# Optimization experiments

Measured on AMD Instinct MI355X. Metric: run time of the kernel, lower is better.

Reference implementation:

```python
import jax, jax.numpy as jnp
import numpy as np

BLOCK_SIZE = 32
BLOCK_COUNTS = 8
N_MAX = 1024  # max seq len across jagged batch (static)
LN_EPS = 1e-5


def _silu(x):
    return x * jax.nn.sigmoid(x)


def setup_inputs() -> dict:
    key = jax.random.key(0)
    ks = jax.random.split(key, 5)
    T, H, D = 3200, 8, 128
    lengths = np.array([1024, 768, 896, 512], dtype=np.int64)
    offsets = np.concatenate([[0], np.cumsum(lengths)]).astype(np.int64)  # [B+1]
    q = jax.random.normal(ks[0], (T, H, D), jnp.float32)
    k = jax.random.normal(ks[1], (T, H, D), jnp.float32)
    v = jax.random.normal(ks[2], (T, H, D), jnp.float32)
    u = jax.random.normal(ks[3], (T, H, D), jnp.float32)
    Wg = jax.random.normal(ks[4], (H, D, 3), jnp.float32) * 0.05
    bg = jnp.zeros((H, 3), jnp.float32)
    return {"q": q, "k": k, "v": v, "u": u, "Wg": Wg, "bg": bg,
            "x_offsets": jnp.asarray(offsets)}


def _to_padded(jag, offsets, lengths, n):
    # jag: [T, H, D] -> [B, n, H, D], zero padded
    pos = jnp.arange(n)
    idx = offsets[:-1, None] + pos[None, :]                # [B, n]
    valid = pos[None, :] < lengths[:, None]                # [B, n]
    g = jag[jnp.clip(idx, 0, jag.shape[0] - 1)]            # [B, n, H, D]
    return jnp.where(valid[..., None, None], g, 0.0)


def _to_jagged(padded, offsets, T):
    tok = jnp.arange(T)
    b = jnp.searchsorted(offsets, tok, side='right') - 1   # batch id per token
    m = tok - offsets[b]                                   # local position
    return padded[b, m]


def _forward(q, k, v, u, Wg, bg, x_offsets):
    T, H, D = q.shape
    B = x_offsets.shape[0] - 1
    n = N_MAX
    bs = BLOCK_SIZE
    nb = n // bs
    S = min(BLOCK_COUNTS, nb)
    scale = D ** (-0.5)
    lengths = x_offsets[1:] - x_offsets[:-1]

    qp = _to_padded(q, x_offsets, lengths, n)  # [B, n, H, D]
    kp = _to_padded(k, x_offsets, lengths, n)
    vp = _to_padded(v, x_offsets, lengths, n)

    # gate model: per-head linear D->3 + sigmoid
    gates = jax.nn.sigmoid(jnp.einsum('bmhd,hde->bmhe', qp, Wg) + bg)
    g_cmp, g_slc = gates[..., 0], gates[..., 1]  # [B, n, H]

    # --- block compression ---
    k_cmp = kp.reshape(B, nb, bs, H, D).mean(axis=2)  # [B, nb, H, D]
    v_cmp = vp.reshape(B, nb, bs, H, D).mean(axis=2)

    # --- compressed attention + top-k block selection ---
    scores = jnp.einsum('bmhd,bkhd->bhmk', qp, k_cmp) * scale  # [B, H, n, nb]
    qblk = jnp.arange(n) // bs
    causal = qblk[:, None] >= jnp.arange(nb)[None, :]          # [n, nb]
    masked_scores = jnp.where(causal[None, None], scores, -jnp.inf)
    _, topk = jax.lax.top_k(masked_scores, S)                  # [B, H, n, S]
    topk = jnp.where(topk > qblk[None, None, :, None], -1, topk)

    p_cmp = jnp.where(causal[None, None], _silu(scores), 0.0)
    o_cmp = jnp.einsum('bhmk,bkhd->bmhd', p_cmp, v_cmp) * g_cmp[..., None]

    # --- selected (gathered top-k block) attention ---
    topk_p = jnp.transpose(topk, (0, 2, 1, 3))                 # [B, n, H, S]
    Kb = kp.reshape(B, nb, bs, H, D).transpose(0, 1, 3, 2, 4)  # [B, nb, H, bs, D]
    Vb = vp.reshape(B, nb, bs, H, D).transpose(0, 1, 3, 2, 4)
    b_ix = jnp.arange(B)[:, None, None]
    h_ix = jnp.arange(H)[None, None, :]
    m_pos = jnp.arange(n)
    off = jnp.arange(bs)

    def body(acc, s_idx):
        blk = jnp.take(topk_p, s_idx, axis=3)                  # [B, n, H]
        blk_c = jnp.maximum(blk, 0)
        Ks = Kb[b_ix, blk_c, h_ix]                             # [B, n, H, bs, D]
        Vs = Vb[b_ix, blk_c, h_ix]
        sc = jnp.einsum('bmhd,bmhkd->bmhk', qp, Ks) * scale    # [B, n, H, bs]
        kpos = blk_c[..., None] * bs + off                     # [B, n, H, bs]
        ok = (blk >= 0)[..., None] & (kpos <= m_pos[None, :, None, None])
        p = jnp.where(ok, _silu(sc), 0.0)
        acc = acc + jnp.einsum('bmhk,bmhkd->bmhd', p, Vs)
        return acc, None

    acc, _ = jax.lax.scan(jax.checkpoint(body), jnp.zeros_like(qp), jnp.arange(S))
    o_slc = acc * g_slc[..., None]

    # back to jagged, LayerNorm over flattened (H*D), gate by u
    o_cmp_j = _to_jagged(o_cmp, x_offsets, T)
    o_slc_j = _to_jagged(o_slc, x_offsets, T)

    def ln_u(x):
        xf = x.reshape(T, H * D)
        mu = xf.mean(-1, keepdims=True)
        var = ((xf - mu) ** 2).mean(-1, keepdims=True)
        xn = (xf - mu) * jax.lax.rsqrt(var + LN_EPS)
        return xn.reshape(T, H, D) * u

    out = ln_u(o_cmp_j) + ln_u(o_slc_j)
    return out, qp, kp


def reference(q, k, v, u, Wg, bg, x_offsets):
    return _forward(q, k, v, u, Wg, bg, x_offsets)
```

## Files before the change

kernel.cpp:

```cpp
#include <hip/hip_runtime.h>
#include <hip/hip_bf16.h>
#include <cmath>

#define H 8
#define D 128
#define HD 1024
#define NMAX 1024
#define BS 32
#define NB 32
#define S_SEL 8
#define CHUNK 8
#define MC 4
#define KP 136
#define SCALE 0.08838834764831845f
#define SENT -3.0e38f

typedef __attribute__((ext_vector_type(8))) short short8;
typedef __attribute__((ext_vector_type(4))) float f32x4;

#define MFMA16(a, b, c) __builtin_amdgcn_mfma_f32_16x16x32_bf16(a, b, c, 0, 0, 0)

__device__ __forceinline__ float silu(float x) {
    return x * __builtin_amdgcn_rcpf(1.f + __expf(-x));
}
__device__ __forceinline__ float sigmoid_fast(float x) {
    return __builtin_amdgcn_rcpf(1.f + __expf(-x));
}
__device__ __forceinline__ unsigned short f2bf(float x) {
    return __builtin_bit_cast(unsigned short, __float2bfloat16(x));
}
__device__ __forceinline__ float bfup(unsigned short b) {
    unsigned u = (unsigned)b << 16;
    return __builtin_bit_cast(float, u);
}
__device__ __forceinline__ void split3(float x, unsigned short& b0,
                                       unsigned short& b1, unsigned short& b2) {
    b0 = f2bf(x);
    float r1 = x - bfup(b0);
    b1 = f2bf(r1);
    float r2 = r1 - bfup(b1);
    b2 = f2bf(r2);
}

__global__ __launch_bounds__(256) void prep_kernel(
    const float* __restrict__ q, const float* __restrict__ k,
    const float* __restrict__ v, const float* __restrict__ Wg,
    const float* __restrict__ bg, const int* __restrict__ offs,
    unsigned short* __restrict__ kb16, unsigned short* __restrict__ vt_blk,
    float* __restrict__ g, unsigned short* __restrict__ kc0,
    unsigned short* __restrict__ kc1, unsigned short* __restrict__ kc2,
    unsigned short* __restrict__ vt_cmp) {
    int x = blockIdx.x;
    int nt = x & (NB - 1);
    int h = (x >> 5) & 7;
    int b = x >> 8;
    int o0 = offs[b];
    int len = offs[b + 1] - o0;
    int tid = threadIdx.x;
    size_t bh = (size_t)(b * H + h);
    if (nt * BS >= len) {
        if (tid < 128) {
            kc0[(bh * NB + nt) * 128 + tid] = 0;
            kc1[(bh * NB + nt) * 128 + tid] = 0;
            kc2[(bh * NB + nt) * 128 + tid] = 0;
            vt_cmp[(bh * 128 + tid) * NB + nt] = 0;
        }
        return;
    }

    __shared__ __align__(16) unsigned short tile[128 * 40];
    __shared__ float redK[4][128];
    __shared__ float redV[4][128];
    int j = tid >> 3, dc = tid & 7;
    int w = tid >> 6, lane = tid & 63;
    size_t base = (size_t)(o0 + nt * BS + j) * HD + h * D + dc * 16;

    {
        float xv[16];
        *(float4*)(xv + 0)  = *(const float4*)(k + base);
        *(float4*)(xv + 4)  = *(const float4*)(k + base + 4);
        *(float4*)(xv + 8)  = *(const float4*)(k + base + 8);
        *(float4*)(xv + 12) = *(const float4*)(k + base + 12);
        short8 lo, hi;
#pragma unroll
        for (int i = 0; i < 8; i++) { lo[i] = (short)f2bf(xv[i]); hi[i] = (short)f2bf(xv[8 + i]); }
        *(short8*)(kb16 + base) = lo;
        *(short8*)(kb16 + base + 8) = hi;
#pragma unroll
        for (int i = 0; i < 16; i++) {
            float s = xv[i];
            s += __shfl_xor(s, 8); s += __shfl_xor(s, 16); s += __shfl_xor(s, 32);
            if (lane < 8) redK[w][lane * 16 + i] = s;
        }
    }
    {
        float xv[16];
        *(float4*)(xv + 0)  = *(const float4*)(v + base);
        *(float4*)(xv + 4)  = *(const float4*)(v + base + 4);
        *(float4*)(xv + 8)  = *(const float4*)(v + base + 8);
        *(float4*)(xv + 12) = *(const float4*)(v + base + 12);
#pragma unroll
        for (int i = 0; i < 16; i++) tile[(dc * 16 + i) * 40 + j] = f2bf(xv[i]);
#pragma unroll
        for (int i = 0; i < 16; i++) {
            float s = xv[i];
            s += __shfl_xor(s, 8); s += __shfl_xor(s, 16); s += __shfl_xor(s, 32);
            if (lane < 8) redV[w][lane * 16 + i] = s;
        }
    }
    {
        float xv[16];
        *(float4*)(xv + 0)  = *(const float4*)(q + base);
        *(float4*)(xv + 4)  = *(const float4*)(q + base + 4);
        *(float4*)(xv + 8)  = *(const float4*)(q + base + 8);
        *(float4*)(xv + 12) = *(const float4*)(q + base + 12);
        float p0 = 0.f, p1 = 0.f;
#pragma unroll
        for (int i = 0; i < 16; i++) {
            int wb = (h * D + dc * 16 + i) * 3;
            p0 += xv[i] * Wg[wb + 0];
            p1 += xv[i] * Wg[wb + 1];
        }
#pragma unroll
        for (int off = 4; off > 0; off >>= 1) {
            p0 += __shfl_xor(p0, off);
            p1 += __shfl_xor(p1, off);
        }
        if (dc == 0) {
            float g0 = sigmoid_fast(p0 + bg[h * 3 + 0]);
            float g1 = sigmoid_fast(p1 + bg[h * 3 + 1]);
            float* gp = g + (size_t)((b * NMAX + nt * BS + j) * H + h) * 2;
            gp[0] = g0; gp[1] = g1;
        }
    }
    __syncthreads();
    {
        int d = tid >> 1, hf = tid & 1;
        short8 a = *(const short8*)(tile + d * 40 + hf * 16);
        short8 c = *(const short8*)(tile + d * 40 + hf * 16 + 8);
        size_t ob = ((bh * NB + nt) * 128 + (size_t)d) * 32 + hf * 16;
        *(short8*)(vt_blk + ob) = a;
        *(short8*)(vt_blk + ob + 8) = c;
    }
    if (tid < 128) {
        int d = tid;
        const float inv = 1.f / 32.f;
        float km = (redK[0][d] + redK[1][d] + redK[2][d] + redK[3][d]) * inv;
        float vm = (redV[0][d] + redV[1][d] + redV[2][d] + redV[3][d]) * inv;
        unsigned short e0, e1, e2;
        split3(km, e0, e1, e2);
        kc0[(bh * NB + nt) * 128 + d] = e0;
        kc1[(bh * NB + nt) * 128 + d] = e1;
        kc2[(bh * NB + nt) * 128 + d] = e2;
        vt_cmp[(bh * 128 + d) * NB + nt] = f2bf(vm);
    }
}

__global__ __launch_bounds__(256) void cmp_attn(
    const float* __restrict__ q, const unsigned short* __restrict__ kc0,
    const unsigned short* __restrict__ kc1, const unsigned short* __restrict__ kc2,
    const unsigned short* __restrict__ vt_cmp, const float* __restrict__ g,
    const int* __restrict__ offs, unsigned* __restrict__ ms_g,
    float* __restrict__ o_cmp_j) {
    int x = blockIdx.x;
    int qblk = (NB - 1) - (x & (NB - 1));
    int h = (x >> 5) & 7;
    int b = x >> 8;
    int o0 = offs[b];
    int len = offs[b + 1] - o0;
    if (qblk * BS >= len) return;
    size_t bh = (size_t)(b * H + h);

    __shared__ __align__(16) unsigned short pool[19456];
    __shared__ float Ss[32 * 33];
    unsigned short* R0 = pool;
    unsigned short* R1 = pool + 4352;
    unsigned short* R2 = pool + 8704;
    unsigned short* R3 = pool + 13056;
    unsigned short* Ps = pool + 18176;

    int tid = threadIdx.x;
    int w = tid >> 6, lane = tid & 63;
    int r = lane & 15, quad = lane >> 4;
    int mt = w >> 1, jt = w & 1;
    int stg_j = tid >> 3, stg_dc = tid & 7;

    if (stg_j <= qblk) {
        size_t src = (bh * NB + stg_j) * 128 + stg_dc * 16;
        int ofs = stg_j * 136 + stg_dc * 16;
        short8 a0 = *(const short8*)(kc0 + src);
        short8 b0 = *(const short8*)(kc0 + src + 8);
        short8 a1 = *(const short8*)(kc1 + src);
        short8 b1 = *(const short8*)(kc1 + src + 8);
        short8 a2 = *(const short8*)(kc2 + src);
        short8 b2 = *(const short8*)(kc2 + src + 8);
        *(short8*)(R0 + ofs) = a0; *(short8*)(R0 + ofs + 8) = b0;
        *(short8*)(R1 + ofs) = a1; *(short8*)(R1 + ofs + 8) = b1;
        *(short8*)(R2 + ofs) = a2; *(short8*)(R2 + ofs + 8) = b2;
    }
    {
        int d = tid >> 1, hf = tid & 1;
        short8 vv = *(const short8*)(vt_cmp + (bh * 128 + d) * NB + hf * 16);
        short8 vw = *(const short8*)(vt_cmp + (bh * 128 + d) * NB + hf * 16 + 8);
        *(short8*)(R3 + d * 40 + hf * 16) = vv;
        *(short8*)(R3 + d * 40 + hf * 16 + 8) = vw;
    }
    __syncthreads();

    f32x4 sv = (f32x4){0.f, 0.f, 0.f, 0.f};
    if (jt == 0 || qblk >= 16) {
        short8 qf0[4], qf1[4], qf2[4];
        const float* qrow = q + (size_t)(o0 + qblk * BS + mt * 16 + r) * HD + h * D;
#pragma unroll
        for (int s = 0; s < 4; s++) {
            const float* p0 = qrow + s * 32 + quad * 8;
            float xv[8];
            *(float4*)(xv) = *(const float4*)p0;
            *(float4*)(xv + 4) = *(const float4*)(p0 + 4);
            short8 f0, f1, f2;
#pragma unroll
            for (int i = 0; i < 8; i++) {
                unsigned short e0, e1, e2;
                split3(xv[i], e0, e1, e2);
                f0[i] = (short)e0; f1[i] = (short)e1; f2[i] = (short)e2;
            }
            qf0[s] = f0; qf1[s] = f1; qf2[s] = f2;
        }
#pragma unroll
        for (int s = 0; s < 4; s++) {
            int ofs = (jt * 16 + r) * 136 + s * 32 + quad * 8;
            short8 k0 = *(const short8*)(R0 + ofs);
            short8 k1 = *(const short8*)(R1 + ofs);
            short8 k2 = *(const short8*)(R2 + ofs);
            sv = MFMA16(qf1[s], k1, sv);
            sv = MFMA16(qf0[s], k2, sv);
            sv = MFMA16(qf2[s], k0, sv);
            sv = MFMA16(qf0[s], k1, sv);
            sv = MFMA16(qf1[s], k0, sv);
            sv = MFMA16(qf0[s], k0, sv);
        }
    }
    int colj = jt * 16 + r;
    bool causal = (colj <= qblk);
#pragma unroll
    for (int i = 0; i < 4; i++) {
        int mrow = mt * 16 + quad * 4 + i;
        float sc = sv[i] * SCALE;
        Ss[mrow * 33 + colj] = causal ? sc : SENT;
        Ps[mrow * 40 + colj] = f2bf(causal ? silu(sc) : 0.f);
    }
    __syncthreads();

    f32x4 accC[2][2];
#pragma unroll
    for (int a = 0; a < 2; a++)
#pragma unroll
        for (int c = 0; c < 2; c++) accC[a][c] = (f32x4){0.f, 0.f, 0.f, 0.f};
    {
        short8 pf0 = *(const short8*)(Ps + r * 40 + quad * 8);
        short8 pf1 = *(const short8*)(Ps + (16 + r) * 40 + quad * 8);
        short8 vf0 = *(const short8*)(R3 + ((2 * w + 0) * 16 + r) * 40 + quad * 8);
        short8 vf1 = *(const short8*)(R3 + ((2 * w + 1) * 16 + r) * 40 + quad * 8);
        accC[0][0] = MFMA16(pf0, vf0, accC[0][0]);
        accC[0][1] = MFMA16(pf0, vf1, accC[0][1]);
        accC[1][0] = MFMA16(pf1, vf0, accC[1][0]);
        accC[1][1] = MFMA16(pf1, vf1, accC[1][1]);
    }
    size_t msbase = (bh << 10) + (size_t)qblk * BS;
    if (qblk < S_SEL) {
        if (tid < BS) ms_g[msbase + tid] = (1u << (qblk + 1)) - 1u;
    } else {
        int h2 = lane >> 5, l32 = lane & 31;
#pragma unroll
        for (int pass = 0; pass < 4; pass++) {
            int row = w * 8 + pass * 2 + h2;
            float val = Ss[row * 33 + l32];
            int cnt = 0;
#pragma unroll
            for (int kk = 1; kk < 32; kk++) {
                int jj = (l32 + kk) & 31;
                float ov = __shfl(val, h2 * 32 + jj);
                if ((ov > val) || (ov == val && jj < l32)) cnt++;
            }
            bool sel = (cnt < S_SEL) && (val > -2.9e38f);
            unsigned long long bal = __ballot(sel);
            unsigned mask = (unsigned)(h2 ? (bal >> 32) : (bal & 0xffffffffULL));
            if (l32 == 0) ms_g[msbase + row] = mask;
        }
    }
#pragma unroll
    for (int mtl = 0; mtl < 2; mtl++) {
#pragma unroll
        for (int i = 0; i < 4; i++) {
            int mrow = mtl * 16 + quad * 4 + i;
            int gm = qblk * BS + mrow;
            float gc = g[(size_t)((b * NMAX + gm) * H + h) * 2];
            float* dst = o_cmp_j + (size_t)(o0 + gm) * HD + h * D;
            dst[(2 * w + 0) * 16 + r] = accC[mtl][0][i] * gc;
            dst[(2 * w + 1) * 16 + r] = accC[mtl][1][i] * gc;
        }
    }
}

__global__ __launch_bounds__(256) void slc_attn(
    const float* __restrict__ q, const unsigned short* __restrict__ kb16,
    const unsigned short* __restrict__ vt_blk, const float* __restrict__ g,
    const int* __restrict__ offs, const unsigned* __restrict__ ms_g,
    float* __restrict__ o_slc_j) {
    int x = blockIdx.x;
    int chunk = x & (MC - 1);
    int mtile = 15 - ((x >> 2) & 15);
    int h = (x >> 6) & 7;
    int b = x >> 9;
    int o0 = offs[b];
    int len = offs[b + 1] - o0;
    if (mtile * 64 >= len) return;
    int qmax = 2 * mtile + 1;
    int kb0 = chunk * CHUNK;
    if (kb0 > qmax) return;
    int kend = min(qmax, kb0 + CHUNK - 1);

    __shared__ __align__(16) unsigned short pool[2 * 32 * KP + 2 * 5120 + 2560];
    __shared__ unsigned Ms[64];
    unsigned short* Kst0 = pool;
    unsigned short* Kst1 = pool + 32 * KP;
    unsigned short* Vst0 = pool + 2 * 32 * KP;
    unsigned short* Vst1 = pool + 2 * 32 * KP + 5120;
    unsigned short* Ps   = pool + 2 * 32 * KP + 10240;

    int tid = threadIdx.x;
    int w = tid >> 6, lane = tid & 63;
    int r = lane & 15, quad = lane >> 4;
    int stg_j = tid >> 3, stg_dc = tid & 7;

    if (tid < 64)
        Ms[tid] = ms_g[((size_t)(b * H + h) << 10) + mtile * 64 + tid];

    short8 qs[4];
    {
        const float* qrow = q + (size_t)(o0 + mtile * 64 + w * 16 + r) * HD + h * D;
#pragma unroll
        for (int s = 0; s < 4; s++) {
            const float* p0 = qrow + s * 32 + quad * 8;
            float xv[8];
            *(float4*)(xv) = *(const float4*)p0;
            *(float4*)(xv + 4) = *(const float4*)(p0 + 4);
            short8 f;
#pragma unroll
            for (int i = 0; i < 8; i++) f[i] = (short)f2bf(xv[i]);
            qs[s] = f;
        }
    }
    f32x4 acc[8];
#pragma unroll
    for (int a = 0; a < 8; a++) acc[a] = (f32x4){0.f, 0.f, 0.f, 0.f};

    size_t vtbase = (size_t)((b * H + h) * NB) * 4096;
    int vd = tid >> 1, vhf = tid & 1;

    {
        const unsigned short* ks = kb16 + (size_t)(o0 + kb0 * BS + stg_j) * HD + h * D + stg_dc * 16;
        short8 k0 = *(const short8*)ks;
        short8 k1 = *(const short8*)(ks + 8);
        *(short8*)(Kst0 + stg_j * KP + stg_dc * 16) = k0;
        *(short8*)(Kst0 + stg_j * KP + stg_dc * 16 + 8) = k1;
        const unsigned short* vs = vt_blk + vtbase + (size_t)kb0 * 4096 + tid * 16;
        short8 v0 = *(const short8*)vs;
        short8 v1 = *(const short8*)(vs + 8);
        *(short8*)(Vst0 + vd * 40 + vhf * 16) = v0;
        *(short8*)(Vst0 + vd * 40 + vhf * 16 + 8) = v1;
    }
    __syncthreads();

    int c = 0;
    for (int kb = kb0; kb <= kend; kb++) {
        short8 pk0, pk1, pv0, pv1;
        bool pf = (kb < kend);
        if (pf) {
            const unsigned short* ks = kb16 + (size_t)(o0 + (kb + 1) * BS + stg_j) * HD + h * D + stg_dc * 16;
            pk0 = *(const short8*)ks;
            pk1 = *(const short8*)(ks + 8);
            const unsigned short* vs = vt_blk + vtbase + (size_t)(kb + 1) * 4096 + tid * 16;
            pv0 = *(const short8*)vs;
            pv1 = *(const short8*)(vs + 8);
        }
        unsigned short* K = c ? Kst1 : Kst0;
        unsigned short* V = c ? Vst1 : Vst0;
        f32x4 s0 = (f32x4){0.f, 0.f, 0.f, 0.f};
        f32x4 s1 = (f32x4){0.f, 0.f, 0.f, 0.f};
#pragma unroll
        for (int s = 0; s < 4; s++) {
            short8 kf0 = *(const short8*)(K + r * KP + s * 32 + quad * 8);
            short8 kf1 = *(const short8*)(K + (16 + r) * KP + s * 32 + quad * 8);
            s0 = MFMA16(qs[s], kf0, s0);
            s1 = MFMA16(qs[s], kf1, s1);
        }
#pragma unroll
        for (int jf = 0; jf < 2; jf++) {
            f32x4 svv = jf ? s1 : s0;
            int colj = jf * 16 + r;
            int kpos = kb * BS + colj;
#pragma unroll
            for (int i = 0; i < 4; i++) {
                int mrow = w * 16 + quad * 4 + i;
                int mpos = mtile * 64 + mrow;
                float p = (((Ms[mrow] >> kb) & 1u) && (kpos <= mpos))
                          ? silu(svv[i] * SCALE) : 0.f;
                Ps[mrow * 40 + colj] = f2bf(p);
            }
        }
        {
            short8 pf8 = *(const short8*)(Ps + (w * 16 + r) * 40 + quad * 8);
#pragma unroll
            for (int nf = 0; nf < 8; nf++) {
                short8 vf = *(const short8*)(V + (nf * 16 + r) * 40 + quad * 8);
                acc[nf] = MFMA16(pf8, vf, acc[nf]);
            }
        }
        if (pf) {
            unsigned short* Kn = c ? Kst0 : Kst1;
            unsigned short* Vn = c ? Vst0 : Vst1;
            *(short8*)(Kn + stg_j * KP + stg_dc * 16) = pk0;
            *(short8*)(Kn + stg_j * KP + stg_dc * 16 + 8) = pk1;
            *(short8*)(Vn + vd * 40 + vhf * 16) = pv0;
            *(short8*)(Vn + vd * 40 + vhf * 16 + 8) = pv1;
        }
        __syncthreads();
        c ^= 1;
    }

    bool single = (qmax < CHUNK);
#pragma unroll
    for (int i = 0; i < 4; i++) {
        int mrow = w * 16 + quad * 4 + i;
        int gm = mtile * 64 + mrow;
        float gs = g[(size_t)((b * NMAX + gm) * H + h) * 2 + 1];
        float* dst = o_slc_j + (size_t)(o0 + gm) * HD + h * D;
#pragma unroll
        for (int nf = 0; nf < 8; nf++) {
            float v0 = acc[nf][i] * gs;
            if (single) dst[nf * 16 + r] = v0;
            else        atomicAdd(dst + nf * 16 + r, v0);
        }
    }
}

__global__ __launch_bounds__(256) void pad_qk_kernel(
    const float* __restrict__ q, const float* __restrict__ k,
    const int* __restrict__ offs,
    float* __restrict__ qp, float* __restrict__ kp) {
    int idx = blockIdx.x * 256 + threadIdx.x;
    int d4 = idx & 31;
    int h  = (idx >> 5) & 7;
    int m  = (idx >> 8) & (NMAX - 1);
    int b  = idx >> 18;
    int o0 = offs[b];
    int len = offs[b + 1] - o0;
    float4 qv = make_float4(0.f, 0.f, 0.f, 0.f);
    float4 kv = qv;
    if (m < len) {
        size_t src = (size_t)(o0 + m) * HD + h * D + d4 * 4;
        qv = *(const float4*)(q + src);
        kv = *(const float4*)(k + src);
    }
    *(float4*)(qp + (size_t)idx * 4) = qv;
    *(float4*)(kp + (size_t)idx * 4) = kv;
}

__global__ __launch_bounds__(256) void ln_combine_kernel(
    const float* __restrict__ oc, const float* __restrict__ os,
    const float* __restrict__ u, float* __restrict__ out) {
    int t = blockIdx.x, tid = threadIdx.x;
    size_t base = (size_t)t * HD;
    float4 xc = *(const float4*)(oc + base + tid * 4);
    float4 xs = *(const float4*)(os + base + tid * 4);
    float4 uu = *(const float4*)(u + base + tid * 4);
    float s_c = xc.x + xc.y + xc.z + xc.w;
    float q_c = xc.x * xc.x + xc.y * xc.y + xc.z * xc.z + xc.w * xc.w;
    float s_s = xs.x + xs.y + xs.z + xs.w;
    float q_s = xs.x * xs.x + xs.y * xs.y + xs.z * xs.z + xs.w * xs.w;
#pragma unroll
    for (int off = 32; off > 0; off >>= 1) {
        s_c += __shfl_xor(s_c, off); q_c += __shfl_xor(q_c, off);
        s_s += __shfl_xor(s_s, off); q_s += __shfl_xor(q_s, off);
    }
    __shared__ float red[4][4];
    int w = tid >> 6, lane = tid & 63;
    if (lane == 0) {
        red[w][0] = s_c; red[w][1] = q_c; red[w][2] = s_s; red[w][3] = q_s;
    }
    __syncthreads();
    float tsc = red[0][0] + red[1][0] + red[2][0] + red[3][0];
    float tqc = red[0][1] + red[1][1] + red[2][1] + red[3][1];
    float tss = red[0][2] + red[1][2] + red[2][2] + red[3][2];
    float tqs = red[0][3] + red[1][3] + red[2][3] + red[3][3];
    const float inv = 1.f / 1024.f;
    float mc = tsc * inv, vc = tqc * inv - mc * mc;
    float ms = tss * inv, vs = tqs * inv - ms * ms;
    float rc = rsqrtf(vc + 1e-5f), rs = rsqrtf(vs + 1e-5f);
    float4 o;
    o.x = ((xc.x - mc) * rc + (xs.x - ms) * rs) * uu.x;
    o.y = ((xc.y - mc) * rc + (xs.y - ms) * rs) * uu.y;
    o.z = ((xc.z - mc) * rc + (xs.z - ms) * rs) * uu.z;
    o.w = ((xc.w - mc) * rc + (xs.w - ms) * rs) * uu.w;
    *(float4*)(out + base + tid * 4) = o;
}

extern "C" void kernel_launch(void* const* d_in, const int* in_sizes, int n_in,
                              void* d_out, int out_size, void* d_ws, size_t ws_size,
                              hipStream_t stream) {
    const float* q  = (const float*)d_in[0];
    const float* k  = (const float*)d_in[1];
    const float* v  = (const float*)d_in[2];
    const float* u  = (const float*)d_in[3];
    const float* Wg = (const float*)d_in[4];
    const float* bg = (const float*)d_in[5];
    const int* offs = (const int*)d_in[6];

    int B = in_sizes[6] - 1;
    int T = in_sizes[0] / HD;

    float* out = (float*)d_out;
    float* qp  = out + (size_t)T * HD;
    float* kp  = qp + (size_t)B * NMAX * HD;

    float* o_cmp_j = out;

    size_t plane = (size_t)B * H * NB * 128;
    char* w = (char*)d_ws;
    unsigned short* kc0 = (unsigned short*)w;  w += plane * 2;
    unsigned short* kc1 = (unsigned short*)w;  w += plane * 2;
    unsigned short* kc2 = (unsigned short*)w;  w += plane * 2;
    unsigned short* vt_cmp = (unsigned short*)w; w += plane * 2;
    float* g     = (float*)w;            w += (size_t)B * NMAX * H * 2 * 4;
    unsigned* ms_g = (unsigned*)w;       w += (size_t)B * H * NMAX * 4;
    float* o_slc_j = (float*)w;          w += (size_t)T * HD * 4;

    size_t kb16_bytes = (size_t)T * HD * 2;
    size_t vt_bytes   = (size_t)B * H * NB * 128 * 32 * 2;
    size_t used = (size_t)(w - (char*)d_ws);
    char* scr = (used + kb16_bytes + vt_bytes <= ws_size) ? w : (char*)kp;
    unsigned short* kb16  = (unsigned short*)scr;
    unsigned short* vt_blk = (unsigned short*)(scr + kb16_bytes);

    int prepBlocks = B * H * NB;
    int cmpAttnBlocks = B * H * NB;
    int slcBlocks  = B * H * 16 * MC;
    int padBlocks  = (B * NMAX * HD / 4) / 256;

    (void)hipMemsetAsync(o_slc_j, 0, (size_t)T * HD * sizeof(float), stream);
    prep_kernel<<<prepBlocks, 256, 0, stream>>>(q, k, v, Wg, bg, offs, kb16, vt_blk,
                                                g, kc0, kc1, kc2, vt_cmp);
    cmp_attn<<<cmpAttnBlocks, 256, 0, stream>>>(q, kc0, kc1, kc2, vt_cmp, g,
                                                offs, ms_g, o_cmp_j);
    slc_attn<<<slcBlocks, 256, 0, stream>>>(q, kb16, vt_blk, g, offs, ms_g, o_slc_j);
    pad_qk_kernel<<<padBlocks, 256, 0, stream>>>(q, k, offs, qp, kp);
    ln_combine_kernel<<<T, 256, 0, stream>>>(o_cmp_j, o_slc_j, u, out);
}
```

Measured before the change: 205.4 us.

## Fuse padding and output zeroing into prep kernel, remap slc_attn blocks per XCD

The prep kernel now writes the zero-padded fp32 qp/kp outputs and zeroes the o_slc accumulator from data it already loads. This removes the separate memset and pad_qk kernel launches and their extra reads of q and k whenever the workspace is large enough. The slc_attn grid index is also remapped so that all blocks of one (batch, head) land on the same XCD, which should improve L2 reuse of K/V tiles. The cost is extra stores inside prep_kernel, and the old pad kernel is kept as a fallback when the workspace is too small.

```diff
diff --git a/kernel.cpp b/kernel.cpp
--- a/kernel.cpp
+++ b/kernel.cpp
@@ -12,6 +12,7 @@
 #define CHUNK 8
 #define MC 4
 #define KP 136
+#define NXCD 8
 #define SCALE 0.08838834764831845f
 #define SENT -3.0e38f
 
@@ -49,7 +50,8 @@
     unsigned short* __restrict__ kb16, unsigned short* __restrict__ vt_blk,
     float* __restrict__ g, unsigned short* __restrict__ kc0,
     unsigned short* __restrict__ kc1, unsigned short* __restrict__ kc2,
-    unsigned short* __restrict__ vt_cmp) {
+    unsigned short* __restrict__ vt_cmp, float* __restrict__ o_slc,
+    float* __restrict__ qp, float* __restrict__ kp) {
     int x = blockIdx.x;
     int nt = x & (NB - 1);
     int h = (x >> 5) & 7;
@@ -58,6 +60,8 @@
     int len = offs[b + 1] - o0;
     int tid = threadIdx.x;
     size_t bh = (size_t)(b * H + h);
+    int j = tid >> 3, dc = tid & 7;
+    size_t pbase = (size_t)((b * NMAX + nt * BS + j)) * HD + h * D + dc * 16;
     if (nt * BS >= len) {
         if (tid < 128) {
             kc0[(bh * NB + nt) * 128 + tid] = 0;
@@ -65,15 +69,28 @@
             kc2[(bh * NB + nt) * 128 + tid] = 0;
             vt_cmp[(bh * 128 + tid) * NB + nt] = 0;
         }
+        if (qp) {
+            float4 z = make_float4(0.f, 0.f, 0.f, 0.f);
+#pragma unroll
+            for (int i = 0; i < 4; i++) {
+                *(float4*)(qp + pbase + i * 4) = z;
+                *(float4*)(kp + pbase + i * 4) = z;
+            }
+        }
         return;
     }
 
     __shared__ __align__(16) unsigned short tile[128 * 40];
     __shared__ float redK[4][128];
     __shared__ float redV[4][128];
-    int j = tid >> 3, dc = tid & 7;
     int w = tid >> 6, lane = tid & 63;
     size_t base = (size_t)(o0 + nt * BS + j) * HD + h * D + dc * 16;
+
+    {
+        float4 z = make_float4(0.f, 0.f, 0.f, 0.f);
+#pragma unroll
+        for (int i = 0; i < 4; i++) *(float4*)(o_slc + base + i * 4) = z;
+    }
 
     {
         float xv[16];
@@ -86,6 +103,10 @@
         for (int i = 0; i < 8; i++) { lo[i] = (short)f2bf(xv[i]); hi[i] = (short)f2bf(xv[8 + i]); }
         *(short8*)(kb16 + base) = lo;
         *(short8*)(kb16 + base + 8) = hi;
+        if (kp) {
+#pragma unroll
+            for (int i = 0; i < 4; i++) *(float4*)(kp + pbase + i * 4) = *(float4*)(xv + i * 4);
+        }
 #pragma unroll
         for (int i = 0; i < 16; i++) {
             float s = xv[i];
@@ -114,6 +135,10 @@
         *(float4*)(xv + 4)  = *(const float4*)(q + base + 4);
         *(float4*)(xv + 8)  = *(const float4*)(q + base + 8);
         *(float4*)(xv + 12) = *(const float4*)(q + base + 12);
+        if (qp) {
+#pragma unroll
+            for (int i = 0; i < 4; i++) *(float4*)(qp + pbase + i * 4) = *(float4*)(xv + i * 4);
+        }
         float p0 = 0.f, p1 = 0.f;
 #pragma unroll
         for (int i = 0; i < 16; i++) {
@@ -308,10 +333,14 @@
     const int* __restrict__ offs, const unsigned* __restrict__ ms_g,
     float* __restrict__ o_slc_j) {
     int x = blockIdx.x;
-    int chunk = x & (MC - 1);
-    int mtile = 15 - ((x >> 2) & 15);
-    int h = (x >> 6) & 7;
-    int b = x >> 9;
+    int xcd = x & (NXCD - 1);
+    int rest = x >> 3;
+    int group = rest >> 6;
+    int inner = rest & 63;
+    int bh = group * NXCD + xcd;
+    int b = bh >> 3, h = bh & 7;
+    int chunk = inner & (MC - 1);
+    int mtile = 15 - (inner >> 2);
     int o0 = offs[b];
     int len = offs[b + 1] - o0;
     if (mtile * 64 >= len) return;
@@ -334,7 +363,7 @@
     int stg_j = tid >> 3, stg_dc = tid & 7;
 
     if (tid < 64)
-        Ms[tid] = ms_g[((size_t)(b * H + h) << 10) + mtile * 64 + tid];
+        Ms[tid] = ms_g[((size_t)bh << 10) + mtile * 64 + tid];
 
     short8 qs[4];
     {
@@ -355,7 +384,7 @@
 #pragma unroll
     for (int a = 0; a < 8; a++) acc[a] = (f32x4){0.f, 0.f, 0.f, 0.f};
 
-    size_t vtbase = (size_t)((b * H + h) * NB) * 4096;
+    size_t vtbase = (size_t)(bh * NB) * 4096;
     int vd = tid >> 1, vhf = tid & 1;
 
     {
@@ -539,7 +568,8 @@
     size_t kb16_bytes = (size_t)T * HD * 2;
     size_t vt_bytes   = (size_t)B * H * NB * 128 * 32 * 2;
     size_t used = (size_t)(w - (char*)d_ws);
-    char* scr = (used + kb16_bytes + vt_bytes <= ws_size) ? w : (char*)kp;
+    bool fused_pad = (used + kb16_bytes + vt_bytes <= ws_size);
+    char* scr = fused_pad ? w : (char*)kp;
     unsigned short* kb16  = (unsigned short*)scr;
     unsigned short* vt_blk = (unsigned short*)(scr + kb16_bytes);
 
@@ -548,12 +578,14 @@
     int slcBlocks  = B * H * 16 * MC;
     int padBlocks  = (B * NMAX * HD / 4) / 256;
 
-    (void)hipMemsetAsync(o_slc_j, 0, (size_t)T * HD * sizeof(float), stream);
     prep_kernel<<<prepBlocks, 256, 0, stream>>>(q, k, v, Wg, bg, offs, kb16, vt_blk,
-                                                g, kc0, kc1, kc2, vt_cmp);
+                                                g, kc0, kc1, kc2, vt_cmp, o_slc_j,
+                                                fused_pad ? qp : nullptr,
+                                                fused_pad ? kp : nullptr);
     cmp_attn<<<cmpAttnBlocks, 256, 0, stream>>>(q, kc0, kc1, kc2, vt_cmp, g,
                                                 offs, ms_g, o_cmp_j);
     slc_attn<<<slcBlocks, 256, 0, stream>>>(q, kb16, vt_blk, g, offs, ms_g, o_slc_j);
-    pad_qk_kernel<<<padBlocks, 256, 0, stream>>>(q, k, offs, qp, kp);
+    if (!fused_pad)
+        pad_qk_kernel<<<padBlocks, 256, 0, stream>>>(q, k, offs, qp, kp);
     ln_combine_kernel<<<T, 256, 0, stream>>>(o_cmp_j, o_slc_j, u, out);
 }
```

New measurement: 199.2 us. -3.0%, faster.
